# Performance work log

Hardware: AMD Instinct MI355X
Metric: run time of the kernel (lower is better)

The kernel has to match this reference:

```python
import jax, jax.numpy as jnp
import numpy as np

B, S, H, I = 4, 2048, 2048, 8192
LN_EPS = 1e-6  # DeepSpeed inference layer-norm epsilon


def setup_inputs() -> dict:
    key = jax.random.key(0)
    ks = jax.random.split(key, 10)
    return {
        "input": jax.random.normal(ks[0], (B, S, H), dtype=jnp.float32),
        "residual": jax.random.normal(ks[1], (B, S, H), dtype=jnp.float32),
        "residual_norm": jax.random.normal(ks[2], (B, S, H), dtype=jnp.float32),
        "bias": jax.random.normal(ks[3], (H,), dtype=jnp.float32) * 0.02,
        "gamma": jnp.ones((H,), dtype=jnp.float32) + jax.random.normal(ks[4], (H,), dtype=jnp.float32) * 0.02,
        "beta": jax.random.normal(ks[5], (H,), dtype=jnp.float32) * 0.02,
        "inter_w": jax.random.normal(ks[6], (H, I), dtype=jnp.float32) * 0.02,
        "inter_b": jax.random.normal(ks[7], (I,), dtype=jnp.float32) * 0.02,
        "output_w": jax.random.normal(ks[8], (I, H), dtype=jnp.float32) * 0.02,
        "output_b": jax.random.normal(ks[9], (H,), dtype=jnp.float32) * 0.02,
    }


def reference(input, residual, residual_norm, bias, gamma, beta,
              inter_w, inter_b, output_w, output_b):
    # --- mlp_gemm_func (pre-LN path, attn_nw is not None) ---
    # Fused: residual_add = attention_output + attention_bias + residual
    residual_add = input + residual + bias                    # [B,S,H]
    # LayerNorm over hidden dim
    mu = jnp.mean(residual_add, axis=-1, keepdims=True)
    var = jnp.mean(jnp.square(residual_add - mu), axis=-1, keepdims=True)
    ln = (residual_add - mu) * jax.lax.rsqrt(var + LN_EPS) * gamma + beta
    # GEMM + bias + GeLU, then second GEMM
    h = jax.nn.gelu(jnp.einsum("bsh,hi->bsi", ln, inter_w) + inter_b,
                    approximate=False)                        # [B,S,I]
    out = jnp.einsum("bsi,ih->bsh", h, output_w)              # [B,S,H]
    # --- residual_add_func (pre-LN, mlp_after_attn): mlp_out + residual_add + final_bias ---
    return out + residual_add + output_b
```

## Files before the change

kernel.cpp:

```cpp
#include <hip/hip_runtime.h>

typedef __attribute__((ext_vector_type(8))) __bf16 bf16x8;
typedef __attribute__((ext_vector_type(4))) float f32x4;

#define AS1(p) ((const __attribute__((address_space(1))) void*)(uintptr_t)(p))
#define AS3(p) ((__attribute__((address_space(3))) void*)(uint32_t)(uintptr_t)(p))
#define GLD16(gp, lp) __builtin_amdgcn_global_load_lds(AS1(gp), AS3(lp), 16, 0, 0)

static constexpr int Bb = 4, Ss = 2048, Hh = 2048, Ih = 8192;
static constexpr int Mm = Bb * Ss;

__device__ __forceinline__ float gelu_exact(float x) {
    return 0.5f * x * (1.0f + erff(x * 0.70710678118654752440f));
}

__global__ __launch_bounds__(256) void transpose_cvt(const float* __restrict__ src,
                                                     __bf16* __restrict__ dst,
                                                     int R, int C) {
    __shared__ float tile[32][33];
    const int tx = threadIdx.x, ty = threadIdx.y;
    const int cB = blockIdx.x * 32, rB = blockIdx.y * 32;
#pragma unroll
    for (int i = 0; i < 4; ++i)
        tile[ty + i * 8][tx] = src[(size_t)(rB + ty + i * 8) * C + cB + tx];
    __syncthreads();
#pragma unroll
    for (int i = 0; i < 4; ++i)
        dst[(size_t)(cB + ty + i * 8) * R + rB + tx] = (__bf16)tile[tx][ty + i * 8];
}

__global__ __launch_bounds__(256) void fused_ln(const float* __restrict__ input,
                                                const float* __restrict__ residual,
                                                const float* __restrict__ bias,
                                                const float* __restrict__ gamma,
                                                const float* __restrict__ beta,
                                                __bf16* __restrict__ lnb,
                                                __bf16* __restrict__ rab) {
    const int row = blockIdx.x;
    const int tid = threadIdx.x;
    const size_t base = (size_t)row * Hh;
    const int e = tid * 8;

    float4 x0 = *(const float4*)(input + base + e);
    float4 x1 = *(const float4*)(input + base + e + 4);
    float4 r0 = *(const float4*)(residual + base + e);
    float4 r1 = *(const float4*)(residual + base + e + 4);
    float4 b0 = *(const float4*)(bias + e);
    float4 b1 = *(const float4*)(bias + e + 4);

    float s[8];
    s[0] = x0.x + r0.x + b0.x; s[1] = x0.y + r0.y + b0.y;
    s[2] = x0.z + r0.z + b0.z; s[3] = x0.w + r0.w + b0.w;
    s[4] = x1.x + r1.x + b1.x; s[5] = x1.y + r1.y + b1.y;
    s[6] = x1.z + r1.z + b1.z; s[7] = x1.w + r1.w + b1.w;

    float sum = 0.f, sq = 0.f;
#pragma unroll
    for (int j = 0; j < 8; ++j) { sum += s[j]; sq += s[j] * s[j]; }
#pragma unroll
    for (int o = 32; o > 0; o >>= 1) {
        sum += __shfl_xor(sum, o);
        sq  += __shfl_xor(sq, o);
    }
    __shared__ float red[8];
    const int wv = tid >> 6, ln_ = tid & 63;
    if (ln_ == 0) { red[wv] = sum; red[4 + wv] = sq; }
    __syncthreads();
    sum = red[0] + red[1] + red[2] + red[3];
    sq  = red[4] + red[5] + red[6] + red[7];

    const float mu   = sum * (1.0f / Hh);
    const float var  = sq * (1.0f / Hh) - mu * mu;
    const float rstd = rsqrtf(var + 1e-6f);

    float4 g0 = *(const float4*)(gamma + e);
    float4 g1 = *(const float4*)(gamma + e + 4);
    float4 t0 = *(const float4*)(beta + e);
    float4 t1 = *(const float4*)(beta + e + 4);
    float g[8] = {g0.x, g0.y, g0.z, g0.w, g1.x, g1.y, g1.z, g1.w};
    float t[8] = {t0.x, t0.y, t0.z, t0.w, t1.x, t1.y, t1.z, t1.w};

    bf16x8 lv, rv;
#pragma unroll
    for (int j = 0; j < 8; ++j) {
        rv[j] = (__bf16)s[j];
        lv[j] = (__bf16)((s[j] - mu) * rstd * g[j] + t[j]);
    }
    *(bf16x8*)(lnb + base + e) = lv;
    *(bf16x8*)(rab + base + e) = rv;
}


#define CFENCE asm volatile("" ::: "memory")
#define BARX   do { CFENCE; __builtin_amdgcn_s_barrier(); CFENCE; } while (0)
#define SP1 __builtin_amdgcn_s_setprio(1)
#define SP0 __builtin_amdgcn_s_setprio(0)
#define VM2 asm volatile("s_waitcnt vmcnt(2)" ::: "memory")
#define VM0 asm volatile("s_waitcnt vmcnt(0)" ::: "memory")

__device__ __forceinline__ void rdA(bf16x8 (&af)[4][2], const char* p0, const char* p1,
                                    const int off) {
#pragma unroll
    for (int m = 0; m < 4; ++m) {
        af[m][0] = *(const bf16x8*)(p0 + off + m * 2048);
        af[m][1] = *(const bf16x8*)(p1 + off + m * 2048);
    }
}
__device__ __forceinline__ void rdB(bf16x8 (&bf)[2][2], const char* p0, const char* p1,
                                    const int off) {
#pragma unroll
    for (int n = 0; n < 2; ++n) {
        bf[n][0] = *(const bf16x8*)(p0 + off + n * 2048);
        bf[n][1] = *(const bf16x8*)(p1 + off + n * 2048);
    }
}
template <int MH, int NH>
__device__ __forceinline__ void mfmaQ(const bf16x8 (&a)[4][2], const bf16x8 (&b)[2][2],
                                      f32x4 (&acc)[8][4]) {
#pragma unroll
    for (int ks = 0; ks < 2; ++ks)
#pragma unroll
        for (int m = 0; m < 4; ++m)
#pragma unroll
            for (int n = 0; n < 2; ++n)
                acc[MH * 4 + m][NH * 2 + n] = __builtin_amdgcn_mfma_f32_16x16x32_bf16(
                    a[m][ks], b[n][ks], acc[MH * 4 + m][NH * 2 + n], 0, 0, 0);
}
__device__ __forceinline__ void stage2(const __bf16* src, __bf16* dst, const size_t row64) {
    GLD16(src, dst);
    GLD16(src + row64, dst + 4096);
}

template <int MODE>
__global__ __launch_bounds__(512, 2) void gemm256(const __bf16* __restrict__ A,
                                                  const __bf16* __restrict__ Bt,
                                                  const float* __restrict__ bias,
                                                  const __bf16* __restrict__ rab,
                                                  __bf16* __restrict__ outH,
                                                  float* __restrict__ outF,
                                                  int M, int N, int K) {
    __shared__ __align__(128) __bf16 lds[2 * 4 * 128 * 64];

    const int tid = threadIdx.x;
    const int nbx = N >> 8;
    const int nwg = gridDim.x;
    const int cpx = nwg >> 3;
    const int bid = blockIdx.x;
    const int swz = (bid & 7) * cpx + (bid >> 3);
    const int by = swz / nbx, bx = swz - by * nbx;
    const int mBase = by << 8, nBase = bx << 8;

    const int wave = tid >> 6, lane = tid & 63;
    const int wr = wave >> 2, wc = wave & 3;

    const int NT = K >> 6;
    const int NI = NT >> 1;

    char* ldsc = (char*)lds;
    const int laneCol0 = (((lane >> 4) << 4)) ^ ((lane & 7) << 4);
    const int laneCol1 = laneCol0 ^ 64;
    const int aLaneR = (lane & 15) << 7;
    const int bLaneR = (((wc & 1) << 6) + (lane & 15)) << 7;
    const char* pA[2][2] = {
        {ldsc + (0 * 4 + wr) * 16384 + aLaneR + laneCol0,
         ldsc + (0 * 4 + wr) * 16384 + aLaneR + laneCol1},
        {ldsc + (1 * 4 + wr) * 16384 + aLaneR + laneCol0,
         ldsc + (1 * 4 + wr) * 16384 + aLaneR + laneCol1}};
    const char* pB[2][2] = {
        {ldsc + (0 * 4 + 2 + (wc >> 1)) * 16384 + bLaneR + laneCol0,
         ldsc + (0 * 4 + 2 + (wc >> 1)) * 16384 + bLaneR + laneCol1},
        {ldsc + (1 * 4 + 2 + (wc >> 1)) * 16384 + bLaneR + laneCol0,
         ldsc + (1 * 4 + 2 + (wc >> 1)) * 16384 + bLaneR + laneCol1}};

    const int srow = tid >> 3;
    const int scol = ((tid & 7) ^ (srow & 7)) << 3;
    const __bf16* aSt = A + (size_t)(mBase + srow) * K + scol;
    const __bf16* bSt = Bt + (size_t)(nBase + srow) * K + scol;
    __bf16* lw = lds + tid * 8;
    const size_t row64 = (size_t)64 * K;
    const size_t row128 = (size_t)128 * K;

#define STA(buf, h, t) stage2(aSt + (h) * row128 + (size_t)(t) * 64, lw + ((buf) * 4 + (h)) * 8192, row64)
#define STB(buf, h, t) stage2(bSt + (h) * row128 + (size_t)(t) * 64, lw + ((buf) * 4 + 2 + (h)) * 8192, row64)

    f32x4 acc[8][4] = {};
    bf16x8 af[4][2], b0[2][2], b1[2][2];

    STA(0, 0, 0); STA(0, 1, 0); STB(0, 0, 0); STB(0, 1, 0);
    VM0;
    BARX;
    STB(1, 0, 1); STB(1, 1, 1);
    rdA(af, pA[0][0], pA[0][1], 0);
    rdB(b0, pB[0][0], pB[0][1], 0);

    for (int i = 0; i < NI; ++i) {
        const int t0 = 2 * i, t1 = 2 * i + 1;
        const bool pf0 = (t0 + 2 < NT);
        const bool pf1 = (t1 + 2 < NT);
        const bool last = (i == NI - 1);

        SP1; mfmaQ<0, 0>(af, b0, acc); SP0;
        rdB(b1, pB[0][0], pB[0][1], 4096);
        STA(1, 0, t1);
        BARX;
        SP1; mfmaQ<0, 1>(af, b1, acc); SP0;
        rdA(af, pA[0][0], pA[0][1], 8192);
        STA(1, 1, t1);
        BARX;
        SP1; mfmaQ<1, 1>(af, b1, acc); SP0;
        if (pf0) { STB(0, 0, t0 + 2); VM2; } else { VM0; }
        BARX;
        SP1; mfmaQ<1, 0>(af, b0, acc); SP0;
        rdA(af, pA[1][0], pA[1][1], 0);
        rdB(b0, pB[1][0], pB[1][1], 0);
        if (pf0) STB(0, 1, t0 + 2);
        BARX;
        SP1; mfmaQ<0, 0>(af, b0, acc); SP0;
        rdB(b1, pB[1][0], pB[1][1], 4096);
        if (pf0) STA(0, 0, t0 + 2);
        BARX;
        SP1; mfmaQ<0, 1>(af, b1, acc); SP0;
        rdA(af, pA[1][0], pA[1][1], 8192);
        if (pf0) STA(0, 1, t0 + 2);
        BARX;
        SP1; mfmaQ<1, 1>(af, b1, acc); SP0;
        if (pf1) { STB(1, 0, t1 + 2); VM2; } else { VM0; }
        BARX;
        SP1; mfmaQ<1, 0>(af, b0, acc); SP0;
        if (!last) {
            rdA(af, pA[0][0], pA[0][1], 0);
            rdB(b0, pB[0][0], pB[0][1], 0);
        }
        if (pf1) STB(1, 1, t1 + 2);
        BARX;
    }

    const int r0 = mBase + wr * 128 + ((lane >> 4) << 2);
    const int c0 = nBase + wc * 64 + (lane & 15);
    float bb[4];
#pragma unroll
    for (int nf = 0; nf < 4; ++nf) bb[nf] = bias[c0 + nf * 16];
#pragma unroll
    for (int mf = 0; mf < 8; ++mf) {
        const int row = r0 + mf * 16;
#pragma unroll
        for (int nf = 0; nf < 4; ++nf) {
            const int col = c0 + nf * 16;
#pragma unroll
            for (int j = 0; j < 4; ++j) {
                const size_t idx = (size_t)(row + j) * N + col;
                const float v = acc[mf][nf][j] + bb[nf];
                if (MODE == 0) {
                    outH[idx] = (__bf16)gelu_exact(v);
                } else {
                    outF[idx] = v + (float)rab[idx];
                }
            }
        }
    }
#undef STA
#undef STB
}

extern "C" void kernel_launch(void* const* d_in, const int* in_sizes, int n_in,
                              void* d_out, int out_size, void* d_ws, size_t ws_size,
                              hipStream_t stream) {
    const float* input    = (const float*)d_in[0];
    const float* residual = (const float*)d_in[1];
    const float* bias     = (const float*)d_in[3];
    const float* gamma    = (const float*)d_in[4];
    const float* beta     = (const float*)d_in[5];
    const float* inter_w  = (const float*)d_in[6];
    const float* inter_b  = (const float*)d_in[7];
    const float* output_w = (const float*)d_in[8];
    const float* output_b = (const float*)d_in[9];
    float* out = (float*)d_out;

    __bf16* w1t  = (__bf16*)d_ws;
    __bf16* w2t  = w1t + (size_t)Ih * Hh;
    __bf16* lnb  = w2t + (size_t)Hh * Ih;
    __bf16* rab  = lnb + (size_t)Mm * Hh;
    __bf16* hbuf = rab + (size_t)Mm * Hh;

    transpose_cvt<<<dim3(Ih / 32, Hh / 32), dim3(32, 8), 0, stream>>>(inter_w, w1t, Hh, Ih);
    transpose_cvt<<<dim3(Hh / 32, Ih / 32), dim3(32, 8), 0, stream>>>(output_w, w2t, Ih, Hh);

    fused_ln<<<Mm, 256, 0, stream>>>(input, residual, bias, gamma, beta, lnb, rab);

    gemm256<0><<<dim3((Mm / 256) * (Ih / 256)), 512, 0, stream>>>(
        lnb, w1t, inter_b, nullptr, hbuf, nullptr, Mm, Ih, Hh);

    gemm256<1><<<dim3((Mm / 256) * (Hh / 256)), 512, 0, stream>>>(
        hbuf, w2t, output_b, rab, nullptr, out, Mm, Hh, Ih);
}
```

Before: 594.9 us.

## Add separate first-GEMM kernel with whole-tile double-buffered prefetch schedule

Splits the templated GEMM into a dedicated GELU GEMM (gemmX) and the residual-output GEMM. The new first-GEMM kernel preloads both LDS buffers up front, waits on vmcnt(0) once per tile, and issues the entire next-next tile's A and B loads in one batch at the end of each tile. The old schedule staggered A and B loads across half-iterations. This restructures load/compute overlap for the K=2048 GEMM, at the risk of a full vmcnt(0) stall mid-tile if the loads have not landed.

```diff
diff --git a/kernel.cpp b/kernel.cpp
--- a/kernel.cpp
+++ b/kernel.cpp
@@ -90,7 +90,6 @@
     *(bf16x8*)(rab + base + e) = rv;
 }
 
-
 #define CFENCE asm volatile("" ::: "memory")
 #define BARX   do { CFENCE; __builtin_amdgcn_s_barrier(); CFENCE; } while (0)
 #define SP1 __builtin_amdgcn_s_setprio(1)
@@ -131,57 +130,116 @@
     GLD16(src + row64, dst + 4096);
 }
 
-template <int MODE>
+#define GEMM_SETUP(Aptr, Btptr)                                                          \
+    const int tid = threadIdx.x;                                                         \
+    const int nbx = N >> 8;                                                              \
+    const int nwg = gridDim.x;                                                           \
+    const int cpx = nwg >> 3;                                                            \
+    const int bid = blockIdx.x;                                                          \
+    const int swz = (bid & 7) * cpx + (bid >> 3);                                        \
+    const int by = swz / nbx, bx = swz - by * nbx;                                       \
+    const int mBase = by << 8, nBase = bx << 8;                                          \
+    const int wave = tid >> 6, lane = tid & 63;                                          \
+    const int wr = wave >> 2, wc = wave & 3;                                             \
+    const int NT = K >> 6;                                                               \
+    const int NI = NT >> 1;                                                              \
+    char* ldsc = (char*)lds;                                                             \
+    const int laneCol0 = (((lane >> 4) << 4)) ^ ((lane & 7) << 4);                       \
+    const int laneCol1 = laneCol0 ^ 64;                                                  \
+    const int aLaneR = (lane & 15) << 7;                                                 \
+    const int bLaneR = (((wc & 1) << 6) + (lane & 15)) << 7;                             \
+    const char* pA[2][2] = {                                                             \
+        {ldsc + (0 * 4 + wr) * 16384 + aLaneR + laneCol0,                                \
+         ldsc + (0 * 4 + wr) * 16384 + aLaneR + laneCol1},                               \
+        {ldsc + (1 * 4 + wr) * 16384 + aLaneR + laneCol0,                                \
+         ldsc + (1 * 4 + wr) * 16384 + aLaneR + laneCol1}};                              \
+    const char* pB[2][2] = {                                                             \
+        {ldsc + (0 * 4 + 2 + (wc >> 1)) * 16384 + bLaneR + laneCol0,                     \
+         ldsc + (0 * 4 + 2 + (wc >> 1)) * 16384 + bLaneR + laneCol1},                    \
+        {ldsc + (1 * 4 + 2 + (wc >> 1)) * 16384 + bLaneR + laneCol0,                     \
+         ldsc + (1 * 4 + 2 + (wc >> 1)) * 16384 + bLaneR + laneCol1}};                   \
+    const int srow = tid >> 3;                                                           \
+    const int scol = ((tid & 7) ^ (srow & 7)) << 3;                                      \
+    const __bf16* aSt = (Aptr) + (size_t)(mBase + srow) * K + scol;                      \
+    const __bf16* bSt = (Btptr) + (size_t)(nBase + srow) * K + scol;                     \
+    __bf16* lw = lds + tid * 8;                                                          \
+    const size_t row64 = (size_t)64 * K;                                                 \
+    const size_t row128 = (size_t)128 * K;
+
+#define STA(buf, h, t) stage2(aSt + (h) * row128 + (size_t)(t) * 64, lw + ((buf) * 4 + (h)) * 8192, row64)
+#define STB(buf, h, t) stage2(bSt + (h) * row128 + (size_t)(t) * 64, lw + ((buf) * 4 + 2 + (h)) * 8192, row64)
+
+__global__ __launch_bounds__(512, 2) void gemmX(const __bf16* __restrict__ A,
+                                                const __bf16* __restrict__ Bt,
+                                                const float* __restrict__ bias,
+                                                __bf16* __restrict__ outH,
+                                                int M, int N, int K) {
+    __shared__ __align__(128) __bf16 lds[2 * 4 * 128 * 64];
+    GEMM_SETUP(A, Bt)
+
+    f32x4 acc[8][4] = {};
+    bf16x8 af[4][2], b0[2][2], b1[2][2];
+
+    STA(0, 0, 0); STA(0, 1, 0); STB(0, 0, 0); STB(0, 1, 0);
+    STA(1, 0, 1); STA(1, 1, 1); STB(1, 0, 1); STB(1, 1, 1);
+    VM0;
+    BARX;
+    rdA(af, pA[0][0], pA[0][1], 0);
+    rdB(b0, pB[0][0], pB[0][1], 0);
+
+#define TILEX(P, NP, BLO, BHI, PF, T2)                          \
+    SP1; mfmaQ<0, 0>(af, BLO, acc); SP0;                        \
+    rdB(BHI, pB[P][0], pB[P][1], 4096);                         \
+    BARX;                                                       \
+    SP1; mfmaQ<0, 1>(af, BHI, acc); SP0;                        \
+    rdA(af, pA[P][0], pA[P][1], 8192);                          \
+    VM0;                                                        \
+    BARX;                                                       \
+    SP1; mfmaQ<1, 1>(af, BHI, acc); SP0;                        \
+    rdB(BHI, pB[NP][0], pB[NP][1], 0);                          \
+    BARX;                                                       \
+    SP1; mfmaQ<1, 0>(af, BLO, acc); SP0;                        \
+    rdA(af, pA[NP][0], pA[NP][1], 0);                           \
+    if (PF) { STA(P, 0, T2); STA(P, 1, T2); STB(P, 0, T2); STB(P, 1, T2); } \
+    BARX;
+
+    for (int i = 0; i < NI; ++i) {
+        const int t0 = 2 * i, t1 = 2 * i + 1;
+        const bool pf0 = (t0 + 2 < NT);
+        const bool pf1 = (t1 + 2 < NT);
+        TILEX(0, 1, b0, b1, pf0, t0 + 2)
+        TILEX(1, 0, b1, b0, pf1, t1 + 2)
+    }
+#undef TILEX
+
+    const int r0 = mBase + wr * 128 + ((lane >> 4) << 2);
+    const int c0 = nBase + wc * 64 + (lane & 15);
+    float bb[4];
+#pragma unroll
+    for (int nf = 0; nf < 4; ++nf) bb[nf] = bias[c0 + nf * 16];
+#pragma unroll
+    for (int mf = 0; mf < 8; ++mf) {
+        const int row = r0 + mf * 16;
+#pragma unroll
+        for (int nf = 0; nf < 4; ++nf) {
+            const int col = c0 + nf * 16;
+#pragma unroll
+            for (int j = 0; j < 4; ++j) {
+                const size_t idx = (size_t)(row + j) * N + col;
+                outH[idx] = (__bf16)gelu_exact(acc[mf][nf][j] + bb[nf]);
+            }
+        }
+    }
+}
+
 __global__ __launch_bounds__(512, 2) void gemm256(const __bf16* __restrict__ A,
                                                   const __bf16* __restrict__ Bt,
                                                   const float* __restrict__ bias,
                                                   const __bf16* __restrict__ rab,
-                                                  __bf16* __restrict__ outH,
                                                   float* __restrict__ outF,
                                                   int M, int N, int K) {
     __shared__ __align__(128) __bf16 lds[2 * 4 * 128 * 64];
-
-    const int tid = threadIdx.x;
-    const int nbx = N >> 8;
-    const int nwg = gridDim.x;
-    const int cpx = nwg >> 3;
-    const int bid = blockIdx.x;
-    const int swz = (bid & 7) * cpx + (bid >> 3);
-    const int by = swz / nbx, bx = swz - by * nbx;
-    const int mBase = by << 8, nBase = bx << 8;
-
-    const int wave = tid >> 6, lane = tid & 63;
-    const int wr = wave >> 2, wc = wave & 3;
-
-    const int NT = K >> 6;
-    const int NI = NT >> 1;
-
-    char* ldsc = (char*)lds;
-    const int laneCol0 = (((lane >> 4) << 4)) ^ ((lane & 7) << 4);
-    const int laneCol1 = laneCol0 ^ 64;
-    const int aLaneR = (lane & 15) << 7;
-    const int bLaneR = (((wc & 1) << 6) + (lane & 15)) << 7;
-    const char* pA[2][2] = {
-        {ldsc + (0 * 4 + wr) * 16384 + aLaneR + laneCol0,
-         ldsc + (0 * 4 + wr) * 16384 + aLaneR + laneCol1},
-        {ldsc + (1 * 4 + wr) * 16384 + aLaneR + laneCol0,
-         ldsc + (1 * 4 + wr) * 16384 + aLaneR + laneCol1}};
-    const char* pB[2][2] = {
-        {ldsc + (0 * 4 + 2 + (wc >> 1)) * 16384 + bLaneR + laneCol0,
-         ldsc + (0 * 4 + 2 + (wc >> 1)) * 16384 + bLaneR + laneCol1},
-        {ldsc + (1 * 4 + 2 + (wc >> 1)) * 16384 + bLaneR + laneCol0,
-         ldsc + (1 * 4 + 2 + (wc >> 1)) * 16384 + bLaneR + laneCol1}};
-
-    const int srow = tid >> 3;
-    const int scol = ((tid & 7) ^ (srow & 7)) << 3;
-    const __bf16* aSt = A + (size_t)(mBase + srow) * K + scol;
-    const __bf16* bSt = Bt + (size_t)(nBase + srow) * K + scol;
-    __bf16* lw = lds + tid * 8;
-    const size_t row64 = (size_t)64 * K;
-    const size_t row128 = (size_t)128 * K;
-
-#define STA(buf, h, t) stage2(aSt + (h) * row128 + (size_t)(t) * 64, lw + ((buf) * 4 + (h)) * 8192, row64)
-#define STB(buf, h, t) stage2(bSt + (h) * row128 + (size_t)(t) * 64, lw + ((buf) * 4 + 2 + (h)) * 8192, row64)
+    GEMM_SETUP(A, Bt)
 
     f32x4 acc[8][4] = {};
     bf16x8 af[4][2], b0[2][2], b1[2][2];
@@ -249,17 +307,10 @@
 #pragma unroll
             for (int j = 0; j < 4; ++j) {
                 const size_t idx = (size_t)(row + j) * N + col;
-                const float v = acc[mf][nf][j] + bb[nf];
-                if (MODE == 0) {
-                    outH[idx] = (__bf16)gelu_exact(v);
-                } else {
-                    outF[idx] = v + (float)rab[idx];
-                }
+                outF[idx] = acc[mf][nf][j] + bb[nf] + (float)rab[idx];
             }
         }
     }
-#undef STA
-#undef STB
 }
 
 extern "C" void kernel_launch(void* const* d_in, const int* in_sizes, int n_in,
@@ -287,9 +338,9 @@
 
     fused_ln<<<Mm, 256, 0, stream>>>(input, residual, bias, gamma, beta, lnb, rab);
 
-    gemm256<0><<<dim3((Mm / 256) * (Ih / 256)), 512, 0, stream>>>(
-        lnb, w1t, inter_b, nullptr, hbuf, nullptr, Mm, Ih, Hh);
-
-    gemm256<1><<<dim3((Mm / 256) * (Hh / 256)), 512, 0, stream>>>(
-        hbuf, w2t, output_b, rab, nullptr, out, Mm, Hh, Ih);
-}
+    gemmX<<<dim3((Mm / 256) * (Ih / 256)), 512, 0, stream>>>(
+        lnb, w1t, inter_b, hbuf, Mm, Ih, Hh);
+
+    gemm256<<<dim3((Mm / 256) * (Hh / 256)), 512, 0, stream>>>(
+        hbuf, w2t, output_b, rab, out, Mm, Hh, Ih);
+}
```

Measured after the change: 599.8 us. No clear change (+0.8%).

## Use 4-wave 256x256 GEMM with 128x128 per-wave tiles for first GEMM

Applied to the files above, without the earlier changes.

Adds a new gemm4w kernel for the LN→intermediate GEMM+GeLU. It uses 256 threads (4 waves), and each wave computes a 128x128 sub-tile with an 8x8 accumulator array, replacing the 8-wave 128x64 per-wave layout. The staging schedule is reworked so that each wave loads its own rows, with a vmcnt(16) wait. The aim is more register-level operand reuse per LDS read and fewer barriers per MFMA, at the cost of much higher register pressure and one workgroup per CU. The second GEMM keeps the existing kernel, now specialised to only its residual output path.

```diff
diff --git a/kernel.cpp b/kernel.cpp
--- a/kernel.cpp
+++ b/kernel.cpp
@@ -90,30 +90,161 @@
     *(bf16x8*)(rab + base + e) = rv;
 }
 
-
 #define CFENCE asm volatile("" ::: "memory")
 #define BARX   do { CFENCE; __builtin_amdgcn_s_barrier(); CFENCE; } while (0)
 #define SP1 __builtin_amdgcn_s_setprio(1)
 #define SP0 __builtin_amdgcn_s_setprio(0)
+#define VM16 asm volatile("s_waitcnt vmcnt(16)" ::: "memory")
 #define VM2 asm volatile("s_waitcnt vmcnt(2)" ::: "memory")
 #define VM0 asm volatile("s_waitcnt vmcnt(0)" ::: "memory")
 
-__device__ __forceinline__ void rdA(bf16x8 (&af)[4][2], const char* p0, const char* p1,
-                                    const int off) {
+__device__ __forceinline__ void rdF4(bf16x8 (&f)[4][2], const char* p0, const char* p1,
+                                     const int off) {
 #pragma unroll
     for (int m = 0; m < 4; ++m) {
-        af[m][0] = *(const bf16x8*)(p0 + off + m * 2048);
-        af[m][1] = *(const bf16x8*)(p1 + off + m * 2048);
-    }
-}
-__device__ __forceinline__ void rdB(bf16x8 (&bf)[2][2], const char* p0, const char* p1,
-                                    const int off) {
+        f[m][0] = *(const bf16x8*)(p0 + off + m * 2048);
+        f[m][1] = *(const bf16x8*)(p1 + off + m * 2048);
+    }
+}
+__device__ __forceinline__ void rdB2(bf16x8 (&bf)[2][2], const char* p0, const char* p1,
+                                     const int off) {
 #pragma unroll
     for (int n = 0; n < 2; ++n) {
         bf[n][0] = *(const bf16x8*)(p0 + off + n * 2048);
         bf[n][1] = *(const bf16x8*)(p1 + off + n * 2048);
     }
 }
+__device__ __forceinline__ void stage2(const __bf16* src, __bf16* dst, const size_t row64) {
+    GLD16(src, dst);
+    GLD16(src + row64, dst + 4096);
+}
+
+template <int MH, int NH>
+__device__ __forceinline__ void mfmaQ4(const bf16x8 (&a)[4][2], const bf16x8 (&b)[4][2],
+                                       f32x4 (&acc)[8][8]) {
+#pragma unroll
+    for (int ks = 0; ks < 2; ++ks)
+#pragma unroll
+        for (int m = 0; m < 4; ++m)
+#pragma unroll
+            for (int n = 0; n < 4; ++n)
+                acc[MH * 4 + m][NH * 4 + n] = __builtin_amdgcn_mfma_f32_16x16x32_bf16(
+                    a[m][ks], b[n][ks], acc[MH * 4 + m][NH * 4 + n], 0, 0, 0);
+}
+
+__global__ __launch_bounds__(256, 1) void gemm4w(const __bf16* __restrict__ A,
+                                                 const __bf16* __restrict__ Bt,
+                                                 const float* __restrict__ bias,
+                                                 __bf16* __restrict__ outH,
+                                                 int M, int N, int K) {
+    __shared__ __align__(128) __bf16 lds[2 * 4 * 128 * 64];
+
+    const int tid = threadIdx.x;
+    const int nbx = N >> 8;
+    const int nwg = gridDim.x;
+    const int cpx = nwg >> 3;
+    const int bid = blockIdx.x;
+    const int swz = (bid & 7) * cpx + (bid >> 3);
+    const int by = swz / nbx, bx = swz - by * nbx;
+    const int mBase = by << 8, nBase = bx << 8;
+
+    const int wave = tid >> 6, lane = tid & 63;
+    const int wr = wave >> 1, wc = wave & 1;
+
+    const int NT = K >> 6;
+
+    char* ldsc = (char*)lds;
+    const int laneCol0 = (((lane >> 4) << 4)) ^ ((lane & 7) << 4);
+    const int laneCol1 = laneCol0 ^ 64;
+    const int laneR = (lane & 15) << 7;
+    const char* pA[2][2] = {
+        {ldsc + (0 * 4 + wr) * 16384 + laneR + laneCol0,
+         ldsc + (0 * 4 + wr) * 16384 + laneR + laneCol1},
+        {ldsc + (1 * 4 + wr) * 16384 + laneR + laneCol0,
+         ldsc + (1 * 4 + wr) * 16384 + laneR + laneCol1}};
+    const char* pB[2][2] = {
+        {ldsc + (0 * 4 + 2 + wc) * 16384 + laneR + laneCol0,
+         ldsc + (0 * 4 + 2 + wc) * 16384 + laneR + laneCol1},
+        {ldsc + (1 * 4 + 2 + wc) * 16384 + laneR + laneCol0,
+         ldsc + (1 * 4 + 2 + wc) * 16384 + laneR + laneCol1}};
+
+    const int sR = lane >> 3;
+    const int sC = ((lane & 7) ^ sR) << 3;
+    const __bf16* aStW = A + (size_t)(mBase + wave * 32 + sR) * K + sC;
+    const __bf16* bStW = Bt + (size_t)(nBase + wave * 32 + sR) * K + sC;
+    __bf16* lwW = lds + wave * 2048 + lane * 8;
+
+#define STA4(buf, h, t)                                                         \
+    _Pragma("unroll")                                                           \
+    for (int i_ = 0; i_ < 4; ++i_)                                              \
+        GLD16(aStW + ((size_t)((h) * 128 + i_ * 8)) * K + (size_t)(t) * 64,     \
+              lwW + ((buf) * 4 + (h)) * 8192 + i_ * 512)
+#define STB4(buf, h, t)                                                         \
+    _Pragma("unroll")                                                           \
+    for (int i_ = 0; i_ < 4; ++i_)                                              \
+        GLD16(bStW + ((size_t)((h) * 128 + i_ * 8)) * K + (size_t)(t) * 64,     \
+              lwW + ((buf) * 4 + 2 + (h)) * 8192 + i_ * 512)
+
+    f32x4 acc[8][8] = {};
+    bf16x8 af[4][2], bv0[4][2], bv1[4][2];
+
+    STA4(0, 0, 0); STA4(0, 1, 0); STB4(0, 0, 0); STB4(0, 1, 0);
+    VM0;
+    BARX;
+    STA4(1, 0, 1); STA4(1, 1, 1); STB4(1, 0, 1); STB4(1, 1, 1);
+    rdF4(af, pA[0][0], pA[0][1], 0);
+    rdF4(bv0, pB[0][0], pB[0][1], 0);
+
+#define TILE4(P, NP, T, PF, LAST)                                               \
+                                                     \
+    SP1; mfmaQ4<0, 0>(af, bv0, acc); SP0;                                       \
+    rdF4(bv1, pB[P][0], pB[P][1], 8192);                                        \
+    BARX;                                                                       \
+           \
+    SP1; mfmaQ4<0, 1>(af, bv1, acc); SP0;                                       \
+    rdF4(af, pA[P][0], pA[P][1], 8192);                                         \
+    BARX;                                                                       \
+           \
+    SP1; mfmaQ4<1, 1>(af, bv1, acc); SP0;                                       \
+    if (PF) { STB4(P, 0, T + 2); STB4(P, 1, T + 2); }                           \
+    BARX;                                                                       \
+           \
+    SP1; mfmaQ4<1, 0>(af, bv0, acc); SP0;                                       \
+    if (PF) { STA4(P, 0, T + 2); STA4(P, 1, T + 2); VM16; } else { VM0; }       \
+    BARX;                                                                       \
+    if (!LAST) {                                                                \
+        rdF4(af, pA[NP][0], pA[NP][1], 0);                                      \
+        rdF4(bv0, pB[NP][0], pB[NP][1], 0);                                     \
+    }
+
+    const int NI = NT >> 1;
+    for (int i = 0; i < NI; ++i) {
+        const int t0 = 2 * i, t1 = 2 * i + 1;
+        TILE4(0, 1, t0, (t0 + 2 < NT), false)
+        TILE4(1, 0, t1, (t1 + 2 < NT), (i == NI - 1))
+    }
+#undef TILE4
+#undef STA4
+#undef STB4
+
+    const int r0 = mBase + wr * 128 + ((lane >> 4) << 2);
+    const int c0 = nBase + wc * 128 + (lane & 15);
+#pragma unroll
+    for (int mf = 0; mf < 8; ++mf) {
+        const int row = r0 + mf * 16;
+#pragma unroll
+        for (int nf = 0; nf < 8; ++nf) {
+            const int col = c0 + nf * 16;
+            const float bb = bias[col];
+#pragma unroll
+            for (int j = 0; j < 4; ++j) {
+                const size_t idx = (size_t)(row + j) * N + col;
+                outH[idx] = (__bf16)gelu_exact(acc[mf][nf][j] + bb);
+            }
+        }
+    }
+}
+
 template <int MH, int NH>
 __device__ __forceinline__ void mfmaQ(const bf16x8 (&a)[4][2], const bf16x8 (&b)[2][2],
                                       f32x4 (&acc)[8][4]) {
@@ -126,17 +257,11 @@
                 acc[MH * 4 + m][NH * 2 + n] = __builtin_amdgcn_mfma_f32_16x16x32_bf16(
                     a[m][ks], b[n][ks], acc[MH * 4 + m][NH * 2 + n], 0, 0, 0);
 }
-__device__ __forceinline__ void stage2(const __bf16* src, __bf16* dst, const size_t row64) {
-    GLD16(src, dst);
-    GLD16(src + row64, dst + 4096);
-}
-
-template <int MODE>
+
 __global__ __launch_bounds__(512, 2) void gemm256(const __bf16* __restrict__ A,
                                                   const __bf16* __restrict__ Bt,
                                                   const float* __restrict__ bias,
                                                   const __bf16* __restrict__ rab,
-                                                  __bf16* __restrict__ outH,
                                                   float* __restrict__ outF,
                                                   int M, int N, int K) {
     __shared__ __align__(128) __bf16 lds[2 * 4 * 128 * 64];
@@ -190,8 +315,8 @@
     VM0;
     BARX;
     STB(1, 0, 1); STB(1, 1, 1);
-    rdA(af, pA[0][0], pA[0][1], 0);
-    rdB(b0, pB[0][0], pB[0][1], 0);
+    rdF4(af, pA[0][0], pA[0][1], 0);
+    rdB2(b0, pB[0][0], pB[0][1], 0);
 
     for (int i = 0; i < NI; ++i) {
         const int t0 = 2 * i, t1 = 2 * i + 1;
@@ -200,27 +325,27 @@
         const bool last = (i == NI - 1);
 
         SP1; mfmaQ<0, 0>(af, b0, acc); SP0;
-        rdB(b1, pB[0][0], pB[0][1], 4096);
+        rdB2(b1, pB[0][0], pB[0][1], 4096);
         STA(1, 0, t1);
         BARX;
         SP1; mfmaQ<0, 1>(af, b1, acc); SP0;
-        rdA(af, pA[0][0], pA[0][1], 8192);
+        rdF4(af, pA[0][0], pA[0][1], 8192);
         STA(1, 1, t1);
         BARX;
         SP1; mfmaQ<1, 1>(af, b1, acc); SP0;
         if (pf0) { STB(0, 0, t0 + 2); VM2; } else { VM0; }
         BARX;
         SP1; mfmaQ<1, 0>(af, b0, acc); SP0;
-        rdA(af, pA[1][0], pA[1][1], 0);
-        rdB(b0, pB[1][0], pB[1][1], 0);
+        rdF4(af, pA[1][0], pA[1][1], 0);
+        rdB2(b0, pB[1][0], pB[1][1], 0);
         if (pf0) STB(0, 1, t0 + 2);
         BARX;
         SP1; mfmaQ<0, 0>(af, b0, acc); SP0;
-        rdB(b1, pB[1][0], pB[1][1], 4096);
+        rdB2(b1, pB[1][0], pB[1][1], 4096);
         if (pf0) STA(0, 0, t0 + 2);
         BARX;
         SP1; mfmaQ<0, 1>(af, b1, acc); SP0;
-        rdA(af, pA[1][0], pA[1][1], 8192);
+        rdF4(af, pA[1][0], pA[1][1], 8192);
         if (pf0) STA(0, 1, t0 + 2);
         BARX;
         SP1; mfmaQ<1, 1>(af, b1, acc); SP0;
@@ -228,12 +353,14 @@
         BARX;
         SP1; mfmaQ<1, 0>(af, b0, acc); SP0;
         if (!last) {
-            rdA(af, pA[0][0], pA[0][1], 0);
-            rdB(b0, pB[0][0], pB[0][1], 0);
+            rdF4(af, pA[0][0], pA[0][1], 0);
+            rdB2(b0, pB[0][0], pB[0][1], 0);
         }
         if (pf1) STB(1, 1, t1 + 2);
         BARX;
     }
+#undef STA
+#undef STB
 
     const int r0 = mBase + wr * 128 + ((lane >> 4) << 2);
     const int c0 = nBase + wc * 64 + (lane & 15);
@@ -249,17 +376,10 @@
 #pragma unroll
             for (int j = 0; j < 4; ++j) {
                 const size_t idx = (size_t)(row + j) * N + col;
-                const float v = acc[mf][nf][j] + bb[nf];
-                if (MODE == 0) {
-                    outH[idx] = (__bf16)gelu_exact(v);
-                } else {
-                    outF[idx] = v + (float)rab[idx];
-                }
+                outF[idx] = acc[mf][nf][j] + bb[nf] + (float)rab[idx];
             }
         }
     }
-#undef STA
-#undef STB
 }
 
 extern "C" void kernel_launch(void* const* d_in, const int* in_sizes, int n_in,
@@ -287,9 +407,9 @@
 
     fused_ln<<<Mm, 256, 0, stream>>>(input, residual, bias, gamma, beta, lnb, rab);
 
-    gemm256<0><<<dim3((Mm / 256) * (Ih / 256)), 512, 0, stream>>>(
-        lnb, w1t, inter_b, nullptr, hbuf, nullptr, Mm, Ih, Hh);
-
-    gemm256<1><<<dim3((Mm / 256) * (Hh / 256)), 512, 0, stream>>>(
-        hbuf, w2t, output_b, rab, nullptr, out, Mm, Hh, Ih);
-}
+    gemm4w<<<dim3((Mm / 256) * (Ih / 256)), 256, 0, stream>>>(
+        lnb, w1t, inter_b, hbuf, Mm, Ih, Hh);
+
+    gemm256<<<dim3((Mm / 256) * (Hh / 256)), 512, 0, stream>>>(
+        hbuf, w2t, output_b, rab, out, Mm, Hh, Ih);
+}
```

After: 689.1 us. 1.16x slower.
